# Performance work log

Hardware: AMD Instinct MI355X
Metric: run time of the kernel (lower is better)

Reference implementation:

```python
import jax, jax.numpy as jnp
import numpy as np

D_MODEL = 256
NUM_HEADS = 4
EPS = 1e-6


def setup_inputs() -> dict:
    key = jax.random.key(0)
    ks = jax.random.split(key, 9)
    B, T, D = 4, 2048, D_MODEL
    scale = 1.0 / np.sqrt(D)
    inp = {
        "x": jax.random.normal(ks[0], (B, T, D), dtype=jnp.float32),
        "Wq": jax.random.normal(ks[1], (D, D), dtype=jnp.float32) * scale,
        "bq": jnp.zeros((D,), dtype=jnp.float32),
        "Wk": jax.random.normal(ks[2], (D, D), dtype=jnp.float32) * scale,
        "bk": jnp.zeros((D,), dtype=jnp.float32),
        "Wv": jax.random.normal(ks[3], (D, D), dtype=jnp.float32) * scale,
        "bv": jnp.zeros((D,), dtype=jnp.float32),
        "Wo": jax.random.normal(ks[4], (D, D), dtype=jnp.float32) * scale,
        "bo": jnp.zeros((D,), dtype=jnp.float32),
    }
    return inp


def _feature_map(a):
    # F.elu(x) + 1.0
    return jax.nn.elu(a) + 1.0


def reference(x, Wq, bq, Wk, bk, Wv, bv, Wo, bo):
    B, T, D = x.shape
    H = NUM_HEADS
    dh = D // H
    Q = _feature_map((x @ Wq + bq).reshape(B, T, H, dh))
    K = _feature_map((x @ Wk + bk).reshape(B, T, H, dh))
    V = (x @ Wv + bv).reshape(B, T, H, dh)
    # outer-product state: (B,T,H,dh,dh), cumulative over time
    KV = jnp.einsum('bthd,bthm->bthdm', K, V)
    S = jnp.cumsum(KV, axis=1)
    Z = jnp.cumsum(K, axis=1)
    out = jnp.einsum('bthd,bthdm->bthm', Q, S)
    denom = jnp.einsum('bthd,bthd->bth', Q, Z)[..., None] + EPS
    out = (out / denom).reshape(B, T, D)
    return out @ Wo + bo
```

## Files before the change

kernel.cpp:

```cpp
#include <hip/hip_runtime.h>
#include <hip/hip_bf16.h>

#define D_MODEL 256
#define NHEADS 4
#define DHEAD 64
#define BATCH 4
#define TSEQ 2048
#define CHUNK 64
#define NCHUNK (TSEQ / CHUNK)
#define NTOK (BATCH * TSEQ)
#define NBH (BATCH * NHEADS)
#define EPSV 1e-6f
#define LSTRF 68

typedef __bf16 bf16x8 __attribute__((ext_vector_type(8)));
typedef float f32x4 __attribute__((ext_vector_type(4)));
typedef unsigned short us8 __attribute__((ext_vector_type(8)));

__device__ __forceinline__ float elu1(float a) {
    return a > 0.0f ? a + 1.0f : __expf(a);
}

__device__ __forceinline__ unsigned short f2bf(float f) {
    __hip_bfloat16 h = __float2bfloat16(f);
    return __builtin_bit_cast(unsigned short, h);
}

__device__ __forceinline__ float bf2f(unsigned short u) {
    return __bfloat162float(__builtin_bit_cast(__hip_bfloat16, u));
}

__device__ __forceinline__ void unpack2(unsigned int u, float& lo, float& hi) {
    lo = __builtin_bit_cast(float, u << 16);
    hi = __builtin_bit_cast(float, u & 0xFFFF0000u);
}

__device__ __forceinline__ void unpack8(uint4 u, float* f) {
    unpack2(u.x, f[0], f[1]);
    unpack2(u.y, f[2], f[3]);
    unpack2(u.z, f[4], f[5]);
    unpack2(u.w, f[6], f[7]);
}

__device__ __forceinline__ bf16x8 frag8(const float* p) {
    const float4 x = *reinterpret_cast<const float4*>(p);
    const float4 y = *reinterpret_cast<const float4*>(p + 4);
    us8 u;
    u[0] = f2bf(x.x); u[1] = f2bf(x.y); u[2] = f2bf(x.z); u[3] = f2bf(x.w);
    u[4] = f2bf(y.x); u[5] = f2bf(y.y); u[6] = f2bf(y.z); u[7] = f2bf(y.w);
    return __builtin_bit_cast(bf16x8, u);
}

__device__ __forceinline__ void gld_lds16(const void* g, void* l) {
    __builtin_amdgcn_global_load_lds(
        (const __attribute__((address_space(1))) void*)g,
        (__attribute__((address_space(3))) void*)l, 16, 0, 0);
}

__global__ __launch_bounds__(256) void convert_kernel(
    const float* __restrict__ x,
    const float* __restrict__ Wq, const float* __restrict__ Wk,
    const float* __restrict__ Wv, const float* __restrict__ Wo,
    unsigned short* __restrict__ xb,
    unsigned short* __restrict__ Wt, unsigned short* __restrict__ Wot)
{
    const int tid = threadIdx.x;
    if (blockIdx.x < NTOK * D_MODEL / 8 / 256) {
        const int i = (blockIdx.x * 256 + tid) * 8;
        const float4 a = *reinterpret_cast<const float4*>(&x[i]);
        const float4 b = *reinterpret_cast<const float4*>(&x[i + 4]);
        ushort4 u0 = { f2bf(a.x), f2bf(a.y), f2bf(a.z), f2bf(a.w) };
        ushort4 u1 = { f2bf(b.x), f2bf(b.y), f2bf(b.z), f2bf(b.w) };
        *reinterpret_cast<ushort4*>(&xb[i]) = u0;
        *reinterpret_cast<ushort4*>(&xb[i + 4]) = u1;
        return;
    }
    __shared__ float Ls[64][65];
    const int bid = blockIdx.x - NTOK * D_MODEL / 8 / 256;
    const int wi = bid >> 4;
    const int ti = bid & 15;
    const int k0 = (ti >> 2) * 64, n0 = (ti & 3) * 64;
    const float* W = wi == 0 ? Wq : wi == 1 ? Wk : wi == 2 ? Wv : Wo;
#pragma unroll
    for (int i = 0; i < 16; ++i) {
        const int idx = i * 256 + tid;
        const int r = idx >> 6, c = idx & 63;
        Ls[r][c] = W[(size_t)(k0 + r) * D_MODEL + n0 + c];
    }
    __syncthreads();
    unsigned short* outp = (wi < 3) ? (Wt + (size_t)(wi * 256 + n0) * D_MODEL + k0)
                                    : (Wot + (size_t)n0 * D_MODEL + k0);
#pragma unroll
    for (int i = 0; i < 16; ++i) {
        const int idx = i * 256 + tid;
        const int rn = idx >> 6, ck = idx & 63;
        outp[(size_t)rn * D_MODEL + ck] = f2bf(Ls[ck][rn]);
    }
}

template<int MODE>
__global__ __launch_bounds__(256) void mfma_gemm_kernel(
    const unsigned short* __restrict__ A,
    const unsigned short* __restrict__ Bt,
    const float* __restrict__ b0, const float* __restrict__ b1,
    const float* __restrict__ b2,
    void* __restrict__ O0, void* __restrict__ O1, void* __restrict__ O2)
{
    __shared__ __align__(16) unsigned short As[64 * 64];
    __shared__ __align__(16) unsigned short Bs[64 * 64];
    const int tid = threadIdx.x;
    const int wave = tid >> 6, lane = tid & 63;
    const int la = lane & 15, q = lane >> 4;

    int mtile, ntile;
    if (MODE == 0) { ntile = blockIdx.x % 12; mtile = blockIdx.x / 12; }
    else           { ntile = blockIdx.x & 3;  mtile = blockIdx.x >> 2; }
    const int m0 = mtile * 64, n0 = ntile * 64;

    const unsigned short* Ab = A  + (size_t)m0 * D_MODEL;
    const unsigned short* Bb = Bt + (size_t)n0 * D_MODEL;

    f32x4 acc[4];
#pragma unroll
    for (int i = 0; i < 4; ++i) acc[i] = (f32x4){0.f, 0.f, 0.f, 0.f};

    for (int k0 = 0; k0 < D_MODEL; k0 += 64) {
#pragma unroll
        for (int i = 0; i < 2; ++i) {
            const int bslot = i * 256 + wave * 64;
            const int slot = bslot + lane;
            const int m = slot >> 3, s = slot & 7;
            const int g = s ^ (m & 7);
            gld_lds16(Ab + (size_t)m * D_MODEL + k0 + g * 8, &As[bslot * 8]);
            gld_lds16(Bb + (size_t)m * D_MODEL + k0 + g * 8, &Bs[bslot * 8]);
        }
        __syncthreads();

        bf16x8 af[2], bfr[4][2];
#pragma unroll
        for (int kh = 0; kh < 2; ++kh) {
            const int g = kh * 4 + q;
            const int m = wave * 16 + la;
            af[kh] = *reinterpret_cast<const bf16x8*>(
                &As[m * 64 + ((g ^ (m & 7)) << 3)]);
#pragma unroll
            for (int ni = 0; ni < 4; ++ni) {
                const int n = ni * 16 + la;
                bfr[ni][kh] = *reinterpret_cast<const bf16x8*>(
                    &Bs[n * 64 + ((g ^ (n & 7)) << 3)]);
            }
        }
#pragma unroll
        for (int ni = 0; ni < 4; ++ni) {
            acc[ni] = __builtin_amdgcn_mfma_f32_16x16x32_bf16(
                af[0], bfr[ni][0], acc[ni], 0, 0, 0);
            acc[ni] = __builtin_amdgcn_mfma_f32_16x16x32_bf16(
                af[1], bfr[ni][1], acc[ni], 0, 0, 0);
        }
        __syncthreads();
    }

#pragma unroll
    for (int ni = 0; ni < 4; ++ni) {
        const int row = m0 + wave * 16 + q * 4;
        const int col = n0 + ni * 16 + la;
        if (MODE == 0) {
            const int which = col >> 8;
            const int cl = col & 255;
            unsigned short* Out = (unsigned short*)
                (which == 0 ? O0 : which == 1 ? O1 : O2);
            const float* bias = which == 0 ? b0 : which == 1 ? b1 : b2;
            const int act = (which < 2);
            const float bv = bias[cl];
#pragma unroll
            for (int r = 0; r < 4; ++r) {
                float v = acc[ni][r] + bv;
                if (act) v = elu1(v);
                Out[(size_t)(row + r) * D_MODEL + cl] = f2bf(v);
            }
        } else {
            float* Out = (float*)O0;
            const float bv = b0[col];
#pragma unroll
            for (int r = 0; r < 4; ++r)
                Out[(size_t)(row + r) * D_MODEL + col] = acc[ni][r] + bv;
        }
    }
}

__global__ __launch_bounds__(256) void chunksum_kernel(
    const unsigned short* __restrict__ Kb, const unsigned short* __restrict__ Vb,
    float* __restrict__ Pt, float* __restrict__ Zc)
{
    __shared__ __align__(16) float Ktf[DHEAD * LSTRF];
    __shared__ __align__(16) float Vtf[DHEAD * LSTRF];
    const int tid = threadIdx.x;
    const int c  = blockIdx.x % NCHUNK;
    const int bh = blockIdx.x / NCHUNK;
    const int b = bh / NHEADS, h = bh % NHEADS;
    const size_t gbase = ((size_t)(b * TSEQ + c * CHUNK)) * D_MODEL + h * DHEAD;

#pragma unroll
    for (int i = 0; i < 2; ++i) {
        const int idx = i * 256 + tid;
        const int t = idx >> 3, e0 = (idx & 7) * 8;
        float kf[8], vf[8];
        unpack8(*reinterpret_cast<const uint4*>(&Kb[gbase + (size_t)t * D_MODEL + e0]), kf);
        unpack8(*reinterpret_cast<const uint4*>(&Vb[gbase + (size_t)t * D_MODEL + e0]), vf);
#pragma unroll
        for (int j = 0; j < 8; ++j) {
            Ktf[(e0 + j) * LSTRF + t] = kf[j];
            Vtf[(e0 + j) * LSTRF + t] = vf[j];
        }
    }
    __syncthreads();

    const int wave = tid >> 6, lane = tid & 63;
    const int la = lane & 15, q = lane >> 4;
    const int wm = (wave >> 1) * 32, wn = (wave & 1) * 32;

    f32x4 acc[2][2];
#pragma unroll
    for (int i = 0; i < 2; ++i)
#pragma unroll
        for (int j = 0; j < 2; ++j) acc[i][j] = (f32x4){0.f, 0.f, 0.f, 0.f};

#pragma unroll
    for (int ks = 0; ks < 2; ++ks) {
        const int ko = ks * 32 + q * 8;
        const bf16x8 a0  = frag8(&Vtf[(wm + la) * LSTRF + ko]);
        const bf16x8 a1  = frag8(&Vtf[(wm + 16 + la) * LSTRF + ko]);
        const bf16x8 bb0 = frag8(&Ktf[(wn + la) * LSTRF + ko]);
        const bf16x8 bb1 = frag8(&Ktf[(wn + 16 + la) * LSTRF + ko]);
        acc[0][0] = __builtin_amdgcn_mfma_f32_16x16x32_bf16(a0, bb0, acc[0][0], 0, 0, 0);
        acc[0][1] = __builtin_amdgcn_mfma_f32_16x16x32_bf16(a0, bb1, acc[0][1], 0, 0, 0);
        acc[1][0] = __builtin_amdgcn_mfma_f32_16x16x32_bf16(a1, bb0, acc[1][0], 0, 0, 0);
        acc[1][1] = __builtin_amdgcn_mfma_f32_16x16x32_bf16(a1, bb1, acc[1][1], 0, 0, 0);
    }

    float* Pb = Pt + (size_t)blockIdx.x * (DHEAD * DHEAD);
#pragma unroll
    for (int mi = 0; mi < 2; ++mi)
#pragma unroll
        for (int ni = 0; ni < 2; ++ni) {
            const int row = wm + mi * 16 + q * 4;
            const int col = wn + ni * 16 + la;
#pragma unroll
            for (int r = 0; r < 4; ++r)
                Pb[(row + r) * DHEAD + col] = acc[mi][ni][r];
        }

    if (tid < DHEAD) {
        float z = 0.f;
        for (int t = 0; t < CHUNK; ++t) z += Ktf[tid * LSTRF + t];
        Zc[(size_t)blockIdx.x * DHEAD + tid] = z;
    }
}

__global__ __launch_bounds__(256) void prefix_kernel(
    float* __restrict__ P, float* __restrict__ Zc)
{
    const int tid = threadIdx.x;
    if (blockIdx.x < NBH * 16) {
        const int bh = blockIdx.x >> 4;
        const int e = ((blockIdx.x & 15) << 8) + tid;
        const size_t base = (size_t)bh * NCHUNK * (DHEAD * DHEAD) + e;
        float v[NCHUNK];
#pragma unroll
        for (int c = 0; c < NCHUNK; ++c) v[c] = P[base + (size_t)c * (DHEAD * DHEAD)];
        float s = 0.f;
#pragma unroll
        for (int c = 0; c < NCHUNK; ++c) {
            const float t = v[c];
            P[base + (size_t)c * (DHEAD * DHEAD)] = s;
            s += t;
        }
    } else {
        const int j = ((int)(blockIdx.x - NBH * 16) << 8) + tid;
        if (j < NBH * DHEAD) {
            const int bh = j >> 6, d = j & 63;
            float v[NCHUNK];
#pragma unroll
            for (int c = 0; c < NCHUNK; ++c) v[c] = Zc[(bh * NCHUNK + c) * DHEAD + d];
            float s = 0.f;
#pragma unroll
            for (int c = 0; c < NCHUNK; ++c) {
                const float t = v[c];
                Zc[(bh * NCHUNK + c) * DHEAD + d] = s;
                s += t;
            }
        }
    }
}

__global__ __launch_bounds__(256) void chunkout_kernel(
    const unsigned short* __restrict__ Qb, const unsigned short* __restrict__ Kb,
    const unsigned short* __restrict__ Vb,
    const float* __restrict__ Pt, const float* __restrict__ Zx,
    unsigned short* __restrict__ Ob)
{
    __shared__ __align__(16) float Qs[CHUNK * LSTRF];
    __shared__ __align__(16) float Ks[CHUNK * LSTRF];
    __shared__ __align__(16) float Vtf[DHEAD * LSTRF];
    __shared__ __align__(16) float At[CHUNK * LSTRF];
    __shared__ float zsh[DHEAD];
    __shared__ float dnm[CHUNK];

    const int tid = threadIdx.x;
    const int c  = blockIdx.x % NCHUNK;
    const int bh = blockIdx.x / NCHUNK;
    const int b = bh / NHEADS, h = bh % NHEADS;
    const size_t gbase = ((size_t)(b * TSEQ + c * CHUNK)) * D_MODEL + h * DHEAD;
    const float* Pp = Pt + (size_t)blockIdx.x * (DHEAD * DHEAD);

#pragma unroll
    for (int i = 0; i < 2; ++i) {
        const int idx = i * 256 + tid;
        const int t = idx >> 3, e0 = (idx & 7) * 8;
        float qf[8], kf[8], vf[8];
        unpack8(*reinterpret_cast<const uint4*>(&Qb[gbase + (size_t)t * D_MODEL + e0]), qf);
        unpack8(*reinterpret_cast<const uint4*>(&Kb[gbase + (size_t)t * D_MODEL + e0]), kf);
        unpack8(*reinterpret_cast<const uint4*>(&Vb[gbase + (size_t)t * D_MODEL + e0]), vf);
        *reinterpret_cast<float4*>(&Qs[t * LSTRF + e0])     = (float4){qf[0], qf[1], qf[2], qf[3]};
        *reinterpret_cast<float4*>(&Qs[t * LSTRF + e0 + 4]) = (float4){qf[4], qf[5], qf[6], qf[7]};
        *reinterpret_cast<float4*>(&Ks[t * LSTRF + e0])     = (float4){kf[0], kf[1], kf[2], kf[3]};
        *reinterpret_cast<float4*>(&Ks[t * LSTRF + e0 + 4]) = (float4){kf[4], kf[5], kf[6], kf[7]};
#pragma unroll
        for (int j = 0; j < 8; ++j)
            Vtf[(e0 + j) * LSTRF + t] = vf[j];
    }
    if (tid < DHEAD)
        zsh[tid] = Zx[((size_t)bh * NCHUNK + c) * DHEAD + tid];
    __syncthreads();

    const int wave = tid >> 6, lane = tid & 63;
    const int la = lane & 15, q = lane >> 4;
    const int wt = (wave >> 1) * 32, wn = (wave & 1) * 32;

    f32x4 acc[2][2];
#pragma unroll
    for (int i = 0; i < 2; ++i)
#pragma unroll
        for (int j = 0; j < 2; ++j) acc[i][j] = (f32x4){0.f, 0.f, 0.f, 0.f};
#pragma unroll
    for (int ks = 0; ks < 2; ++ks) {
        const int ko = ks * 32 + q * 8;
        const bf16x8 a0  = frag8(&Qs[(wt + la) * LSTRF + ko]);
        const bf16x8 a1  = frag8(&Qs[(wt + 16 + la) * LSTRF + ko]);
        const bf16x8 bb0 = frag8(&Ks[(wn + la) * LSTRF + ko]);
        const bf16x8 bb1 = frag8(&Ks[(wn + 16 + la) * LSTRF + ko]);
        acc[0][0] = __builtin_amdgcn_mfma_f32_16x16x32_bf16(a0, bb0, acc[0][0], 0, 0, 0);
        acc[0][1] = __builtin_amdgcn_mfma_f32_16x16x32_bf16(a0, bb1, acc[0][1], 0, 0, 0);
        acc[1][0] = __builtin_amdgcn_mfma_f32_16x16x32_bf16(a1, bb0, acc[1][0], 0, 0, 0);
        acc[1][1] = __builtin_amdgcn_mfma_f32_16x16x32_bf16(a1, bb1, acc[1][1], 0, 0, 0);
    }
#pragma unroll
    for (int mi = 0; mi < 2; ++mi)
#pragma unroll
        for (int ni = 0; ni < 2; ++ni) {
            const int t0 = wt + mi * 16 + q * 4;
            const int s  = wn + ni * 16 + la;
#pragma unroll
            for (int r = 0; r < 4; ++r)
                At[(t0 + r) * LSTRF + s] = (s <= t0 + r) ? acc[mi][ni][r] : 0.f;
        }
    __syncthreads();

    if (tid < CHUNK) {
        float dv = 0.f;
        for (int s = 0; s < CHUNK; ++s) dv += At[tid * LSTRF + s];
        for (int d = 0; d < DHEAD; ++d) dv = fmaf(Qs[tid * LSTRF + d], zsh[d], dv);
        dnm[tid] = dv + EPSV;
    }
    __syncthreads();

    f32x4 o[2][2];
#pragma unroll
    for (int i = 0; i < 2; ++i)
#pragma unroll
        for (int j = 0; j < 2; ++j) o[i][j] = (f32x4){0.f, 0.f, 0.f, 0.f};
#pragma unroll
    for (int ks = 0; ks < 2; ++ks) {
        const int ko = ks * 32 + q * 8;
        const bf16x8 a0  = frag8(&Qs[(wt + la) * LSTRF + ko]);
        const bf16x8 a1  = frag8(&Qs[(wt + 16 + la) * LSTRF + ko]);
        const bf16x8 bb0 = frag8(&Pp[(wn + la) * DHEAD + ko]);
        const bf16x8 bb1 = frag8(&Pp[(wn + 16 + la) * DHEAD + ko]);
        o[0][0] = __builtin_amdgcn_mfma_f32_16x16x32_bf16(a0, bb0, o[0][0], 0, 0, 0);
        o[0][1] = __builtin_amdgcn_mfma_f32_16x16x32_bf16(a0, bb1, o[0][1], 0, 0, 0);
        o[1][0] = __builtin_amdgcn_mfma_f32_16x16x32_bf16(a1, bb0, o[1][0], 0, 0, 0);
        o[1][1] = __builtin_amdgcn_mfma_f32_16x16x32_bf16(a1, bb1, o[1][1], 0, 0, 0);
    }
#pragma unroll
    for (int ks = 0; ks < 2; ++ks) {
        const int ko = ks * 32 + q * 8;
        const bf16x8 a0  = frag8(&At[(wt + la) * LSTRF + ko]);
        const bf16x8 a1  = frag8(&At[(wt + 16 + la) * LSTRF + ko]);
        const bf16x8 bb0 = frag8(&Vtf[(wn + la) * LSTRF + ko]);
        const bf16x8 bb1 = frag8(&Vtf[(wn + 16 + la) * LSTRF + ko]);
        o[0][0] = __builtin_amdgcn_mfma_f32_16x16x32_bf16(a0, bb0, o[0][0], 0, 0, 0);
        o[0][1] = __builtin_amdgcn_mfma_f32_16x16x32_bf16(a0, bb1, o[0][1], 0, 0, 0);
        o[1][0] = __builtin_amdgcn_mfma_f32_16x16x32_bf16(a1, bb0, o[1][0], 0, 0, 0);
        o[1][1] = __builtin_amdgcn_mfma_f32_16x16x32_bf16(a1, bb1, o[1][1], 0, 0, 0);
    }

#pragma unroll
    for (int mi = 0; mi < 2; ++mi)
#pragma unroll
        for (int ni = 0; ni < 2; ++ni) {
            const int t0 = wt + mi * 16 + q * 4;
            const int m  = wn + ni * 16 + la;
#pragma unroll
            for (int r = 0; r < 4; ++r) {
                const float v = o[mi][ni][r] / dnm[t0 + r];
                Ob[gbase + (size_t)(t0 + r) * D_MODEL + m] = f2bf(v);
            }
        }
}

extern "C" void kernel_launch(void* const* d_in, const int* in_sizes, int n_in,
                              void* d_out, int out_size, void* d_ws, size_t ws_size,
                              hipStream_t stream)
{
    const float* x  = (const float*)d_in[0];
    const float* Wq = (const float*)d_in[1];
    const float* bq = (const float*)d_in[2];
    const float* Wk = (const float*)d_in[3];
    const float* bk = (const float*)d_in[4];
    const float* Wv = (const float*)d_in[5];
    const float* bv = (const float*)d_in[6];
    const float* Wo = (const float*)d_in[7];
    const float* bo = (const float*)d_in[8];
    float* out = (float*)d_out;

    const size_t NE = (size_t)NTOK * D_MODEL;
    unsigned short* xb  = (unsigned short*)d_ws;
    unsigned short* Wt  = xb + NE;
    unsigned short* Wot = Wt + 768 * 256;
    unsigned short* Qb  = Wot + 256 * 256;
    unsigned short* Kb  = Qb + NE;
    unsigned short* Vb  = Kb + NE;
    unsigned short* Ob  = Vb + NE;
    float* P = (float*)(Ob + NE);
    float* Z = P + (size_t)NBH * NCHUNK * DHEAD * DHEAD;

    convert_kernel<<<NTOK * D_MODEL / 8 / 256 + 64, 256, 0, stream>>>(
        x, Wq, Wk, Wv, Wo, xb, Wt, Wot);
    mfma_gemm_kernel<0><<<(NTOK / 64) * 12, 256, 0, stream>>>(
        xb, Wt, bq, bk, bv, Qb, Kb, Vb);
    chunksum_kernel<<<NBH * NCHUNK, 256, 0, stream>>>(Kb, Vb, P, Z);
    prefix_kernel<<<NBH * 16 + 4, 256, 0, stream>>>(P, Z);
    chunkout_kernel<<<NBH * NCHUNK, 256, 0, stream>>>(Qb, Kb, Vb, P, Z, Ob);
    mfma_gemm_kernel<1><<<(NTOK / 64) * 4, 256, 0, stream>>>(
        Ob, Wot, bo, nullptr, nullptr, out, nullptr, nullptr);
}
```

Baseline: 111.6 us.

## Fuse all stages into one persistent cooperative kernel with grid syncs

Replaces the six separate kernel launches (convert, QKV GEMM, chunk sums, prefix scan, chunk output, output GEMM) with a single persistent cooperative kernel. The stages are separated by grid.sync barriers and the blocks loop over work items, with the grid sized by occupancy. The aim is to remove per-launch overhead and launch gaps between stages. In exchange, every stage now runs on a fixed persistent grid, and the prefix stage has few work items, so many blocks sit idle at the barriers. The separate-launch path is kept as a fallback if the cooperative launch fails.

```diff
diff --git a/kernel.cpp b/kernel.cpp
--- a/kernel.cpp
+++ b/kernel.cpp
@@ -1,5 +1,8 @@
 #include <hip/hip_runtime.h>
 #include <hip/hip_bf16.h>
+#include <hip/hip_cooperative_groups.h>
+
+namespace cg = cooperative_groups;
 
 #define D_MODEL 256
 #define NHEADS 4
@@ -55,6 +58,415 @@
     __builtin_amdgcn_global_load_lds(
         (const __attribute__((address_space(1))) void*)g,
         (__attribute__((address_space(3))) void*)l, 16, 0, 0);
+}
+
+__global__ __launch_bounds__(256, 2) void mega_kernel(
+    const float* __restrict__ x,
+    const float* __restrict__ Wq, const float* __restrict__ bq,
+    const float* __restrict__ Wk, const float* __restrict__ bk,
+    const float* __restrict__ Wv, const float* __restrict__ bv,
+    const float* __restrict__ Wo, const float* __restrict__ bo,
+    unsigned short* __restrict__ xb,
+    unsigned short* __restrict__ Wt, unsigned short* __restrict__ Wot,
+    unsigned short* __restrict__ Qb, unsigned short* __restrict__ Kb,
+    unsigned short* __restrict__ Vb,
+    float* __restrict__ P, float* __restrict__ Z,
+    unsigned short* __restrict__ Ob, float* __restrict__ out)
+{
+    __shared__ __align__(16) char pool[52736];
+    cg::grid_group grid = cg::this_grid();
+    const int tid = threadIdx.x;
+    const int nblk = gridDim.x;
+    const int wave = tid >> 6, lane = tid & 63;
+    const int la = lane & 15, q = lane >> 4;
+
+    for (int u = blockIdx.x; u < 1024; u += nblk) {
+        const int i = (u * 256 + tid) * 8;
+        const float4 a = *reinterpret_cast<const float4*>(&x[i]);
+        const float4 b = *reinterpret_cast<const float4*>(&x[i + 4]);
+        ushort4 u0 = { f2bf(a.x), f2bf(a.y), f2bf(a.z), f2bf(a.w) };
+        ushort4 u1 = { f2bf(b.x), f2bf(b.y), f2bf(b.z), f2bf(b.w) };
+        *reinterpret_cast<ushort4*>(&xb[i]) = u0;
+        *reinterpret_cast<ushort4*>(&xb[i + 4]) = u1;
+    }
+    for (int w = blockIdx.x; w < 64; w += nblk) {
+        float (*Ls)[65] = reinterpret_cast<float(*)[65]>(pool);
+        const int wi = w >> 4, ti = w & 15;
+        const int k0 = (ti >> 2) * 64, n0 = (ti & 3) * 64;
+        const float* W = wi == 0 ? Wq : wi == 1 ? Wk : wi == 2 ? Wv : Wo;
+#pragma unroll
+        for (int i = 0; i < 16; ++i) {
+            const int idx = i * 256 + tid;
+            const int r = idx >> 6, c = idx & 63;
+            Ls[r][c] = W[(size_t)(k0 + r) * D_MODEL + n0 + c];
+        }
+        __syncthreads();
+        unsigned short* outp = (wi < 3)
+            ? (Wt + (size_t)(wi * 256 + n0) * D_MODEL + k0)
+            : (Wot + (size_t)n0 * D_MODEL + k0);
+#pragma unroll
+        for (int i = 0; i < 16; ++i) {
+            const int idx = i * 256 + tid;
+            const int rn = idx >> 6, ck = idx & 63;
+            outp[(size_t)rn * D_MODEL + ck] = f2bf(Ls[ck][rn]);
+        }
+        __syncthreads();
+    }
+    __threadfence();
+    grid.sync();
+
+    {
+        unsigned short* As = reinterpret_cast<unsigned short*>(pool);
+        unsigned short* Bs = As + 64 * 64;
+        for (int tt = blockIdx.x; tt < 1536; tt += nblk) {
+            const int ntile = tt % 12, mtile = tt / 12;
+            const int m0 = mtile * 64, n0 = ntile * 64;
+            const unsigned short* Ab = xb + (size_t)m0 * D_MODEL;
+            const unsigned short* Bb = Wt + (size_t)n0 * D_MODEL;
+
+            f32x4 acc[4];
+#pragma unroll
+            for (int i = 0; i < 4; ++i) acc[i] = (f32x4){0.f, 0.f, 0.f, 0.f};
+
+            for (int k0 = 0; k0 < D_MODEL; k0 += 64) {
+#pragma unroll
+                for (int i = 0; i < 2; ++i) {
+                    const int bslot = i * 256 + wave * 64;
+                    const int slot = bslot + lane;
+                    const int m = slot >> 3, s = slot & 7;
+                    const int g = s ^ (m & 7);
+                    gld_lds16(Ab + (size_t)m * D_MODEL + k0 + g * 8, &As[bslot * 8]);
+                    gld_lds16(Bb + (size_t)m * D_MODEL + k0 + g * 8, &Bs[bslot * 8]);
+                }
+                __syncthreads();
+
+                bf16x8 af[2], bfr[4][2];
+#pragma unroll
+                for (int kh = 0; kh < 2; ++kh) {
+                    const int g = kh * 4 + q;
+                    const int m = wave * 16 + la;
+                    af[kh] = *reinterpret_cast<const bf16x8*>(
+                        &As[m * 64 + ((g ^ (m & 7)) << 3)]);
+#pragma unroll
+                    for (int ni = 0; ni < 4; ++ni) {
+                        const int n = ni * 16 + la;
+                        bfr[ni][kh] = *reinterpret_cast<const bf16x8*>(
+                            &Bs[n * 64 + ((g ^ (n & 7)) << 3)]);
+                    }
+                }
+#pragma unroll
+                for (int ni = 0; ni < 4; ++ni) {
+                    acc[ni] = __builtin_amdgcn_mfma_f32_16x16x32_bf16(
+                        af[0], bfr[ni][0], acc[ni], 0, 0, 0);
+                    acc[ni] = __builtin_amdgcn_mfma_f32_16x16x32_bf16(
+                        af[1], bfr[ni][1], acc[ni], 0, 0, 0);
+                }
+                __syncthreads();
+            }
+#pragma unroll
+            for (int ni = 0; ni < 4; ++ni) {
+                const int row = m0 + wave * 16 + q * 4;
+                const int col = n0 + ni * 16 + la;
+                const int which = col >> 8;
+                const int cl = col & 255;
+                unsigned short* Out = which == 0 ? Qb : which == 1 ? Kb : Vb;
+                const float* bias = which == 0 ? bq : which == 1 ? bk : bv;
+                const int act = (which < 2);
+                const float bv2 = bias[cl];
+#pragma unroll
+                for (int r = 0; r < 4; ++r) {
+                    float v = acc[ni][r] + bv2;
+                    if (act) v = elu1(v);
+                    Out[(size_t)(row + r) * D_MODEL + cl] = f2bf(v);
+                }
+            }
+        }
+    }
+    __threadfence();
+    grid.sync();
+
+    {
+        float* Ktf = reinterpret_cast<float*>(pool);
+        float* Vtf = Ktf + DHEAD * LSTRF;
+        for (int t2 = blockIdx.x; t2 < 512; t2 += nblk) {
+            const int c  = t2 % NCHUNK;
+            const int bh = t2 / NCHUNK;
+            const int b = bh / NHEADS, h = bh % NHEADS;
+            const size_t gbase = ((size_t)(b * TSEQ + c * CHUNK)) * D_MODEL + h * DHEAD;
+
+#pragma unroll
+            for (int i = 0; i < 2; ++i) {
+                const int idx = i * 256 + tid;
+                const int t = idx >> 3, e0 = (idx & 7) * 8;
+                float kf[8], vf[8];
+                unpack8(*reinterpret_cast<const uint4*>(&Kb[gbase + (size_t)t * D_MODEL + e0]), kf);
+                unpack8(*reinterpret_cast<const uint4*>(&Vb[gbase + (size_t)t * D_MODEL + e0]), vf);
+#pragma unroll
+                for (int j = 0; j < 8; ++j) {
+                    Ktf[(e0 + j) * LSTRF + t] = kf[j];
+                    Vtf[(e0 + j) * LSTRF + t] = vf[j];
+                }
+            }
+            __syncthreads();
+
+            const int wm = (wave >> 1) * 32, wn = (wave & 1) * 32;
+            f32x4 acc[2][2];
+#pragma unroll
+            for (int i = 0; i < 2; ++i)
+#pragma unroll
+                for (int j = 0; j < 2; ++j) acc[i][j] = (f32x4){0.f, 0.f, 0.f, 0.f};
+#pragma unroll
+            for (int ks = 0; ks < 2; ++ks) {
+                const int ko = ks * 32 + q * 8;
+                const bf16x8 a0  = frag8(&Vtf[(wm + la) * LSTRF + ko]);
+                const bf16x8 a1  = frag8(&Vtf[(wm + 16 + la) * LSTRF + ko]);
+                const bf16x8 bb0 = frag8(&Ktf[(wn + la) * LSTRF + ko]);
+                const bf16x8 bb1 = frag8(&Ktf[(wn + 16 + la) * LSTRF + ko]);
+                acc[0][0] = __builtin_amdgcn_mfma_f32_16x16x32_bf16(a0, bb0, acc[0][0], 0, 0, 0);
+                acc[0][1] = __builtin_amdgcn_mfma_f32_16x16x32_bf16(a0, bb1, acc[0][1], 0, 0, 0);
+                acc[1][0] = __builtin_amdgcn_mfma_f32_16x16x32_bf16(a1, bb0, acc[1][0], 0, 0, 0);
+                acc[1][1] = __builtin_amdgcn_mfma_f32_16x16x32_bf16(a1, bb1, acc[1][1], 0, 0, 0);
+            }
+
+            float* Pb = P + (size_t)t2 * (DHEAD * DHEAD);
+#pragma unroll
+            for (int mi = 0; mi < 2; ++mi)
+#pragma unroll
+                for (int ni = 0; ni < 2; ++ni) {
+                    const int row = wm + mi * 16 + q * 4;
+                    const int col = wn + ni * 16 + la;
+#pragma unroll
+                    for (int r = 0; r < 4; ++r)
+                        Pb[(row + r) * DHEAD + col] = acc[mi][ni][r];
+                }
+
+            if (tid < DHEAD) {
+                float z = 0.f;
+                for (int t = 0; t < CHUNK; ++t) z += Ktf[tid * LSTRF + t];
+                Z[(size_t)t2 * DHEAD + tid] = z;
+            }
+            __syncthreads();
+        }
+    }
+    __threadfence();
+    grid.sync();
+
+    for (int p3 = blockIdx.x; p3 < NBH * 16 + 4; p3 += nblk) {
+        if (p3 < NBH * 16) {
+            const int bh = p3 >> 4;
+            const int e = ((p3 & 15) << 8) + tid;
+            const size_t base = (size_t)bh * NCHUNK * (DHEAD * DHEAD) + e;
+            float v[NCHUNK];
+#pragma unroll
+            for (int c = 0; c < NCHUNK; ++c) v[c] = P[base + (size_t)c * (DHEAD * DHEAD)];
+            float s = 0.f;
+#pragma unroll
+            for (int c = 0; c < NCHUNK; ++c) {
+                const float t = v[c];
+                P[base + (size_t)c * (DHEAD * DHEAD)] = s;
+                s += t;
+            }
+        } else {
+            const int j = ((p3 - NBH * 16) << 8) + tid;
+            if (j < NBH * DHEAD) {
+                const int bh = j >> 6, d = j & 63;
+                float v[NCHUNK];
+#pragma unroll
+                for (int c = 0; c < NCHUNK; ++c) v[c] = Z[(bh * NCHUNK + c) * DHEAD + d];
+                float s = 0.f;
+#pragma unroll
+                for (int c = 0; c < NCHUNK; ++c) {
+                    const float t = v[c];
+                    Z[(bh * NCHUNK + c) * DHEAD + d] = s;
+                    s += t;
+                }
+            }
+        }
+    }
+    __threadfence();
+    grid.sync();
+
+    {
+        float* Qs   = reinterpret_cast<float*>(pool);
+        float* KsAt = Qs + CHUNK * LSTRF;
+        float* Vtf  = KsAt + CHUNK * LSTRF;
+        float* zsh  = Vtf + DHEAD * LSTRF;
+        float* dnm  = zsh + DHEAD;
+
+        for (int t4 = blockIdx.x; t4 < 512; t4 += nblk) {
+            const int c  = t4 % NCHUNK;
+            const int bh = t4 / NCHUNK;
+            const int b = bh / NHEADS, h = bh % NHEADS;
+            const size_t gbase = ((size_t)(b * TSEQ + c * CHUNK)) * D_MODEL + h * DHEAD;
+            const float* Pp = P + (size_t)t4 * (DHEAD * DHEAD);
+
+#pragma unroll
+            for (int i = 0; i < 2; ++i) {
+                const int idx = i * 256 + tid;
+                const int t = idx >> 3, e0 = (idx & 7) * 8;
+                float qf[8], kf[8], vf[8];
+                unpack8(*reinterpret_cast<const uint4*>(&Qb[gbase + (size_t)t * D_MODEL + e0]), qf);
+                unpack8(*reinterpret_cast<const uint4*>(&Kb[gbase + (size_t)t * D_MODEL + e0]), kf);
+                unpack8(*reinterpret_cast<const uint4*>(&Vb[gbase + (size_t)t * D_MODEL + e0]), vf);
+                *reinterpret_cast<float4*>(&Qs[t * LSTRF + e0])       = (float4){qf[0], qf[1], qf[2], qf[3]};
+                *reinterpret_cast<float4*>(&Qs[t * LSTRF + e0 + 4])   = (float4){qf[4], qf[5], qf[6], qf[7]};
+                *reinterpret_cast<float4*>(&KsAt[t * LSTRF + e0])     = (float4){kf[0], kf[1], kf[2], kf[3]};
+                *reinterpret_cast<float4*>(&KsAt[t * LSTRF + e0 + 4]) = (float4){kf[4], kf[5], kf[6], kf[7]};
+#pragma unroll
+                for (int j = 0; j < 8; ++j)
+                    Vtf[(e0 + j) * LSTRF + t] = vf[j];
+            }
+            if (tid < DHEAD)
+                zsh[tid] = Z[((size_t)bh * NCHUNK + c) * DHEAD + tid];
+            __syncthreads();
+
+            const int wt = (wave >> 1) * 32, wn = (wave & 1) * 32;
+
+            f32x4 acc[2][2];
+#pragma unroll
+            for (int i = 0; i < 2; ++i)
+#pragma unroll
+                for (int j = 0; j < 2; ++j) acc[i][j] = (f32x4){0.f, 0.f, 0.f, 0.f};
+#pragma unroll
+            for (int ks = 0; ks < 2; ++ks) {
+                const int ko = ks * 32 + q * 8;
+                const bf16x8 a0  = frag8(&Qs[(wt + la) * LSTRF + ko]);
+                const bf16x8 a1  = frag8(&Qs[(wt + 16 + la) * LSTRF + ko]);
+                const bf16x8 bb0 = frag8(&KsAt[(wn + la) * LSTRF + ko]);
+                const bf16x8 bb1 = frag8(&KsAt[(wn + 16 + la) * LSTRF + ko]);
+                acc[0][0] = __builtin_amdgcn_mfma_f32_16x16x32_bf16(a0, bb0, acc[0][0], 0, 0, 0);
+                acc[0][1] = __builtin_amdgcn_mfma_f32_16x16x32_bf16(a0, bb1, acc[0][1], 0, 0, 0);
+                acc[1][0] = __builtin_amdgcn_mfma_f32_16x16x32_bf16(a1, bb0, acc[1][0], 0, 0, 0);
+                acc[1][1] = __builtin_amdgcn_mfma_f32_16x16x32_bf16(a1, bb1, acc[1][1], 0, 0, 0);
+            }
+            __syncthreads();
+#pragma unroll
+            for (int mi = 0; mi < 2; ++mi)
+#pragma unroll
+                for (int ni = 0; ni < 2; ++ni) {
+                    const int t0 = wt + mi * 16 + q * 4;
+                    const int s  = wn + ni * 16 + la;
+#pragma unroll
+                    for (int r = 0; r < 4; ++r)
+                        KsAt[(t0 + r) * LSTRF + s] = (s <= t0 + r) ? acc[mi][ni][r] : 0.f;
+                }
+            __syncthreads();
+
+            if (tid < CHUNK) {
+                float dv = 0.f;
+                for (int s = 0; s < CHUNK; ++s) dv += KsAt[tid * LSTRF + s];
+                for (int d = 0; d < DHEAD; ++d) dv = fmaf(Qs[tid * LSTRF + d], zsh[d], dv);
+                dnm[tid] = dv + EPSV;
+            }
+            __syncthreads();
+
+            f32x4 o[2][2];
+#pragma unroll
+            for (int i = 0; i < 2; ++i)
+#pragma unroll
+                for (int j = 0; j < 2; ++j) o[i][j] = (f32x4){0.f, 0.f, 0.f, 0.f};
+#pragma unroll
+            for (int ks = 0; ks < 2; ++ks) {
+                const int ko = ks * 32 + q * 8;
+                const bf16x8 a0  = frag8(&Qs[(wt + la) * LSTRF + ko]);
+                const bf16x8 a1  = frag8(&Qs[(wt + 16 + la) * LSTRF + ko]);
+                const bf16x8 bb0 = frag8(&Pp[(wn + la) * DHEAD + ko]);
+                const bf16x8 bb1 = frag8(&Pp[(wn + 16 + la) * DHEAD + ko]);
+                o[0][0] = __builtin_amdgcn_mfma_f32_16x16x32_bf16(a0, bb0, o[0][0], 0, 0, 0);
+                o[0][1] = __builtin_amdgcn_mfma_f32_16x16x32_bf16(a0, bb1, o[0][1], 0, 0, 0);
+                o[1][0] = __builtin_amdgcn_mfma_f32_16x16x32_bf16(a1, bb0, o[1][0], 0, 0, 0);
+                o[1][1] = __builtin_amdgcn_mfma_f32_16x16x32_bf16(a1, bb1, o[1][1], 0, 0, 0);
+            }
+#pragma unroll
+            for (int ks = 0; ks < 2; ++ks) {
+                const int ko = ks * 32 + q * 8;
+                const bf16x8 a0  = frag8(&KsAt[(wt + la) * LSTRF + ko]);
+                const bf16x8 a1  = frag8(&KsAt[(wt + 16 + la) * LSTRF + ko]);
+                const bf16x8 bb0 = frag8(&Vtf[(wn + la) * LSTRF + ko]);
+                const bf16x8 bb1 = frag8(&Vtf[(wn + 16 + la) * LSTRF + ko]);
+                o[0][0] = __builtin_amdgcn_mfma_f32_16x16x32_bf16(a0, bb0, o[0][0], 0, 0, 0);
+                o[0][1] = __builtin_amdgcn_mfma_f32_16x16x32_bf16(a0, bb1, o[0][1], 0, 0, 0);
+                o[1][0] = __builtin_amdgcn_mfma_f32_16x16x32_bf16(a1, bb0, o[1][0], 0, 0, 0);
+                o[1][1] = __builtin_amdgcn_mfma_f32_16x16x32_bf16(a1, bb1, o[1][1], 0, 0, 0);
+            }
+
+#pragma unroll
+            for (int mi = 0; mi < 2; ++mi)
+#pragma unroll
+                for (int ni = 0; ni < 2; ++ni) {
+                    const int t0 = wt + mi * 16 + q * 4;
+                    const int m  = wn + ni * 16 + la;
+#pragma unroll
+                    for (int r = 0; r < 4; ++r) {
+                        const float v = o[mi][ni][r] / dnm[t0 + r];
+                        Ob[gbase + (size_t)(t0 + r) * D_MODEL + m] = f2bf(v);
+                    }
+                }
+            __syncthreads();
+        }
+    }
+    __threadfence();
+    grid.sync();
+
+    {
+        unsigned short* As = reinterpret_cast<unsigned short*>(pool);
+        unsigned short* Bs = As + 64 * 64;
+        for (int tt = blockIdx.x; tt < 512; tt += nblk) {
+            const int ntile = tt & 3, mtile = tt >> 2;
+            const int m0 = mtile * 64, n0 = ntile * 64;
+            const unsigned short* Ab = Ob  + (size_t)m0 * D_MODEL;
+            const unsigned short* Bb = Wot + (size_t)n0 * D_MODEL;
+
+            f32x4 acc[4];
+#pragma unroll
+            for (int i = 0; i < 4; ++i) acc[i] = (f32x4){0.f, 0.f, 0.f, 0.f};
+
+            for (int k0 = 0; k0 < D_MODEL; k0 += 64) {
+#pragma unroll
+                for (int i = 0; i < 2; ++i) {
+                    const int bslot = i * 256 + wave * 64;
+                    const int slot = bslot + lane;
+                    const int m = slot >> 3, s = slot & 7;
+                    const int g = s ^ (m & 7);
+                    gld_lds16(Ab + (size_t)m * D_MODEL + k0 + g * 8, &As[bslot * 8]);
+                    gld_lds16(Bb + (size_t)m * D_MODEL + k0 + g * 8, &Bs[bslot * 8]);
+                }
+                __syncthreads();
+
+                bf16x8 af[2], bfr[4][2];
+#pragma unroll
+                for (int kh = 0; kh < 2; ++kh) {
+                    const int g = kh * 4 + q;
+                    const int m = wave * 16 + la;
+                    af[kh] = *reinterpret_cast<const bf16x8*>(
+                        &As[m * 64 + ((g ^ (m & 7)) << 3)]);
+#pragma unroll
+                    for (int ni = 0; ni < 4; ++ni) {
+                        const int n = ni * 16 + la;
+                        bfr[ni][kh] = *reinterpret_cast<const bf16x8*>(
+                            &Bs[n * 64 + ((g ^ (n & 7)) << 3)]);
+                    }
+                }
+#pragma unroll
+                for (int ni = 0; ni < 4; ++ni) {
+                    acc[ni] = __builtin_amdgcn_mfma_f32_16x16x32_bf16(
+                        af[0], bfr[ni][0], acc[ni], 0, 0, 0);
+                    acc[ni] = __builtin_amdgcn_mfma_f32_16x16x32_bf16(
+                        af[1], bfr[ni][1], acc[ni], 0, 0, 0);
+                }
+                __syncthreads();
+            }
+#pragma unroll
+            for (int ni = 0; ni < 4; ++ni) {
+                const int row = m0 + wave * 16 + q * 4;
+                const int col = n0 + ni * 16 + la;
+                const float bv2 = bo[col];
+#pragma unroll
+                for (int r = 0; r < 4; ++r)
+                    out[(size_t)(row + r) * D_MODEL + col] = acc[ni][r] + bv2;
+            }
+        }
+    }
 }
 
 __global__ __launch_bounds__(256) void convert_kernel(
@@ -77,8 +489,7 @@
     }
     __shared__ float Ls[64][65];
     const int bid = blockIdx.x - NTOK * D_MODEL / 8 / 256;
-    const int wi = bid >> 4;
-    const int ti = bid & 15;
+    const int wi = bid >> 4, ti = bid & 15;
     const int k0 = (ti >> 2) * 64, n0 = (ti & 3) * 64;
     const float* W = wi == 0 ? Wq : wi == 1 ? Wk : wi == 2 ? Wv : Wo;
 #pragma unroll
@@ -444,13 +855,34 @@
     float* P = (float*)(Ob + NE);
     float* Z = P + (size_t)NBH * NCHUNK * DHEAD * DHEAD;
 
-    convert_kernel<<<NTOK * D_MODEL / 8 / 256 + 64, 256, 0, stream>>>(
-        x, Wq, Wk, Wv, Wo, xb, Wt, Wot);
-    mfma_gemm_kernel<0><<<(NTOK / 64) * 12, 256, 0, stream>>>(
-        xb, Wt, bq, bk, bv, Qb, Kb, Vb);
-    chunksum_kernel<<<NBH * NCHUNK, 256, 0, stream>>>(Kb, Vb, P, Z);
-    prefix_kernel<<<NBH * 16 + 4, 256, 0, stream>>>(P, Z);
-    chunkout_kernel<<<NBH * NCHUNK, 256, 0, stream>>>(Qb, Kb, Vb, P, Z, Ob);
-    mfma_gemm_kernel<1><<<(NTOK / 64) * 4, 256, 0, stream>>>(
-        Ob, Wot, bo, nullptr, nullptr, out, nullptr, nullptr);
-}
+    bool coop_ok = false;
+    int occ = 0;
+    hipError_t e = hipOccupancyMaxActiveBlocksPerMultiprocessor(
+        &occ, mega_kernel, 256, 0);
+    if (e == hipSuccess && occ > 0) {
+        int grid = occ * 256;
+        if (grid > 1536) grid = 1536;
+        void* args[] = {
+            (void*)&x, (void*)&Wq, (void*)&bq, (void*)&Wk, (void*)&bk,
+            (void*)&Wv, (void*)&bv, (void*)&Wo, (void*)&bo,
+            (void*)&xb, (void*)&Wt, (void*)&Wot,
+            (void*)&Qb, (void*)&Kb, (void*)&Vb,
+            (void*)&P, (void*)&Z, (void*)&Ob, (void*)&out
+        };
+        e = hipLaunchCooperativeKernel((const void*)mega_kernel,
+                                       dim3(grid), dim3(256), args, 0, stream);
+        coop_ok = (e == hipSuccess);
+    }
+
+    if (!coop_ok) {
+        convert_kernel<<<NTOK * D_MODEL / 8 / 256 + 64, 256, 0, stream>>>(
+            x, Wq, Wk, Wv, Wo, xb, Wt, Wot);
+        mfma_gemm_kernel<0><<<(NTOK / 64) * 12, 256, 0, stream>>>(
+            xb, Wt, bq, bk, bv, Qb, Kb, Vb);
+        chunksum_kernel<<<NBH * NCHUNK, 256, 0, stream>>>(Kb, Vb, P, Z);
+        prefix_kernel<<<NBH * 16 + 4, 256, 0, stream>>>(P, Z);
+        chunkout_kernel<<<NBH * NCHUNK, 256, 0, stream>>>(Qb, Kb, Vb, P, Z, Ob);
+        mfma_gemm_kernel<1><<<(NTOK / 64) * 4, 256, 0, stream>>>(
+            Ob, Wot, bo, nullptr, nullptr, out, nullptr, nullptr);
+    }
+}
```

Measured after the change: 432.2 us. +287.4%, slower.
